# Kernel optimization log

Measured on AMD Instinct MI355X. Metric: run time of the kernel, lower is better.

The kernel has to match this reference:

```python
import jax, jax.numpy as jnp
import numpy as np

H, N, DIN, DOUT = 8, 2048, 768, 1024
HD = DOUT // H
SCALE = 1.0 / float(np.sqrt(HD))
NEG = -1e9
EPS = 1e-5


def setup_inputs() -> dict:
    key = jax.random.key(0)
    ks = jax.random.split(key, 20)
    w = lambda i, shape: jax.random.normal(ks[i], shape, jnp.float32) * 0.02
    inp = {
        'x': jax.random.normal(ks[0], (N, DIN), jnp.float32),
        'batch': jnp.sort(jax.random.randint(ks[1], (N,), 0, 64)).astype(jnp.int64)
                 if jax.config.jax_enable_x64 else jnp.sort(jax.random.randint(ks[1], (N,), 0, 64)),
        'motif_to_atom_attn': jax.random.normal(ks[2], (H, N, N), jnp.float32),
        'wq_w': w(3, (DIN, DOUT)), 'wq_b': jnp.zeros((DOUT,), jnp.float32),
        'wk_w': w(4, (DIN, DOUT)), 'wk_b': jnp.zeros((DOUT,), jnp.float32),
        'wv_w': w(5, (DIN, DOUT)), 'wv_b': jnp.zeros((DOUT,), jnp.float32),
        'wo_w': w(6, (DOUT, DIN)), 'wo_b': jnp.zeros((DIN,), jnp.float32),
        'ln_g': jnp.ones((DIN,), jnp.float32), 'ln_b': jnp.zeros((DIN,), jnp.float32),
        'alpha': jnp.float32(0.5), 'beta': jnp.float32(0.5),
        'gate_q_w': w(7, (DOUT, H)), 'gate_q_b': jnp.zeros((H,), jnp.float32),
        'gate_k_w': w(8, (DOUT, H)), 'gate_k_b': jnp.zeros((H,), jnp.float32),
        'head_interaction': jnp.eye(H, dtype=jnp.float32) + 0.01 * jax.random.normal(ks[9], (H, H), jnp.float32),
    }
    return inp


def reference(x, batch, motif_to_atom_attn, wq_w, wq_b, wk_w, wk_b, wv_w, wv_b,
              wo_w, wo_b, ln_g, ln_b, alpha, beta, gate_q_w, gate_q_b,
              gate_k_w, gate_k_b, head_interaction):
    n = x.shape[0]
    # projections -> [H, N, hd]
    q = (x @ wq_w + wq_b).reshape(n, H, HD).transpose(1, 0, 2)
    k = (x @ wk_w + wk_b).reshape(n, H, HD).transpose(1, 0, 2)
    v = (x @ wv_w + wv_b).reshape(n, H, HD).transpose(1, 0, 2)
    # scaled scores with block-diagonal batch mask [H, N, N]
    scores = jnp.einsum('hid,hjd->hij', q, k) * SCALE
    mask = batch[:, None] == batch[None, :]
    scores = jnp.where(mask[None, :, :], scores, NEG)
    attn_final = scores
    # Guide bias: torch permutes (N,N,H)->permute(2,1,0) which TRANSPOSES node dims
    attn_base = alpha * scores + beta * motif_to_atom_attn          # [H, N, N]
    attn_final = attn_final + jnp.swapaxes(attn_base, 1, 2)        # transposed in (i,j)
    # dynamic gating
    q_flat = q.transpose(1, 0, 2).reshape(n, DOUT)
    k_flat = k.transpose(1, 0, 2).reshape(n, DOUT)
    gq = jnp.tanh(q_flat @ gate_q_w + gate_q_b)                    # [N, H]
    gk = jnp.tanh(k_flat @ gate_k_w + gate_k_b)                    # [N, H]
    attn_final = attn_final + scores * (gq.T[:, :, None] + gk.T[:, None, :])
    # head interaction: res[m,i,j] = sum_h scores[h,i,j] * W[h,m]
    attn_final = attn_final + jnp.einsum('hij,hm->mij', scores, head_interaction)
    probs = jax.nn.softmax(attn_final, axis=-1)
    out = jnp.einsum('hij,hjd->hid', probs, v).transpose(1, 0, 2).reshape(n, DOUT)
    out = out @ wo_w + wo_b
    y = out + x
    mu = jnp.mean(y, axis=-1, keepdims=True)
    var = jnp.mean(jnp.square(y - mu), axis=-1, keepdims=True)
    y = (y - mu) * jax.lax.rsqrt(var + EPS) * ln_g + ln_b
    return y, attn_final
```

## Files before the change

### kernel.cpp

```cpp
#include <hip/hip_runtime.h>

#define NN    2048
#define DIN   768
#define DOUT  1024
#define NH    8
#define HD    128
#define SCALEF 0.08838834764831845f
#define NEGF  (-1.0e9f)
#define EPSF  1e-5f
#define EXPSHIFT 16.0f

typedef __attribute__((ext_vector_type(4))) float f32x4;
typedef __attribute__((ext_vector_type(8))) short bf16x8;

#define OFF_OBF  0
#define OFF_WOT  1048576
#define OFF_YACC 1441792
#define OFF_Q    3686400
#define OFF_K    4734976
#define OFF_VB   5783552
#define OFF_VT   6832128
#define OFF_XB   7880704
#define OFF_WT   8667136
#define OFF_GQ   9846784
#define OFF_GK   9863168

__device__ __forceinline__ short f2bf(float f) {
  union { float f; unsigned u; } v; v.f = f;
  unsigned r = v.u + 0x7FFF + ((v.u >> 16) & 1);
  return (short)(r >> 16);
}
__device__ __forceinline__ float bf2f(short s) {
  union { unsigned u; float f; } v; v.u = ((unsigned)(unsigned short)s) << 16;
  return v.f;
}

__global__ __launch_bounds__(256) void k_prep(const float* __restrict__ x,
                                              short* __restrict__ xb,
                                              const float* __restrict__ wq,
                                              const float* __restrict__ wk,
                                              const float* __restrict__ wv,
                                              short* __restrict__ Wt,
                                              const float* __restrict__ wo,
                                              short* __restrict__ wot) {
  const int bid = blockIdx.x;
  const int tid = threadIdx.x;
  if (bid < 1536) {
    int idx = bid * 256 + tid;
    float4 v = ((const float4*)x)[idx];
    union { short s[4]; float2 f; } u;
    u.s[0] = f2bf(v.x); u.s[1] = f2bf(v.y); u.s[2] = f2bf(v.z); u.s[3] = f2bf(v.w);
    ((float2*)xb)[idx] = u.f;
    return;
  }
  __shared__ float t[64][65];
  if (bid < 2112) {
    const int w = bid - 1536;
    const int z = w / 192, rem = w % 192;
    const int c0 = (rem % 16) * 64, k0 = (rem / 16) * 64;
    const float* Wm = (z == 0) ? wq : (z == 1) ? wk : wv;
#pragma unroll
    for (int l = 0; l < 4; ++l) {
      int f = tid + l * 256;
      int r = f >> 4, c4 = (f & 15) * 4;
      *(float4*)&t[r][c4] = *(const float4*)(Wm + (size_t)(k0 + r) * DOUT + c0 + c4);
    }
    __syncthreads();
    int r2 = tid >> 2, q = tid & 3;
    union { short s[16]; float4 f[2]; } buf;
#pragma unroll
    for (int jj = 0; jj < 16; ++jj) buf.s[jj] = f2bf(t[q * 16 + jj][r2]);
    short* dst = Wt + (size_t)z * (1024 * 768) + (size_t)(c0 + r2) * 768 + k0 + q * 16;
    ((float4*)dst)[0] = buf.f[0];
    ((float4*)dst)[1] = buf.f[1];
  } else {
    const int w = bid - 2112;
    const int c0 = (w % 12) * 64, k0 = (w / 12) * 64;
#pragma unroll
    for (int l = 0; l < 4; ++l) {
      int f = tid + l * 256;
      int r = f >> 4, c4 = (f & 15) * 4;
      *(float4*)&t[r][c4] = *(const float4*)(wo + (size_t)(k0 + r) * DIN + c0 + c4);
    }
    __syncthreads();
    int r2 = tid >> 2, q = tid & 3;
    union { short s[16]; float4 f[2]; } buf;
#pragma unroll
    for (int jj = 0; jj < 16; ++jj) buf.s[jj] = f2bf(t[q * 16 + jj][r2]);
    short* dst = wot + (size_t)(c0 + r2) * DOUT + k0 + q * 16;
    ((float4*)dst)[0] = buf.f[0];
    ((float4*)dst)[1] = buf.f[1];
  }
}

__global__ __launch_bounds__(256) void k_qkv(const short* __restrict__ xb,
                                             const short* __restrict__ Wt,
                                             const float* __restrict__ bq,
                                             const float* __restrict__ bk,
                                             const float* __restrict__ bv,
                                             short* __restrict__ Qb,
                                             short* __restrict__ Kb,
                                             short* __restrict__ Vb) {
  const int n0 = blockIdx.x * 128;
  const int i0 = blockIdx.y * 64;
  const int mat = n0 >> 10;
  const int cl = n0 & 1023;
  const float* bias = (mat == 0) ? bq : (mat == 1) ? bk : bv;
  const short* Wm = Wt + (size_t)mat * (1024 * 768);
  const int tid = threadIdx.x, lane = tid & 63, wave = tid >> 6;
  const int ln = lane & 15, quad = lane >> 4, q8 = quad * 8;
  __shared__ __align__(16) short Bs[2][128][56];
  const int brow = tid >> 1, bseg = (tid & 1) * 16;
  const short* gB = Wm + (size_t)(cl + brow) * DIN + bseg;
  {
    bf16x8 b0 = *(const bf16x8*)(gB);
    bf16x8 b1 = *(const bf16x8*)(gB + 8);
    *(bf16x8*)&Bs[0][brow][bseg] = b0;
    *(bf16x8*)&Bs[0][brow][bseg + 8] = b1;
  }
  bf16x8 cb0 = *(const bf16x8*)(gB + 32);
  bf16x8 cb1 = *(const bf16x8*)(gB + 40);
  __syncthreads();
  f32x4 acc[8];
#pragma unroll
  for (int nt = 0; nt < 8; ++nt) acc[nt] = (f32x4){0.f, 0.f, 0.f, 0.f};
  const short* a0 = xb + (size_t)(i0 + 16 * wave + ln) * DIN + q8;
  for (int ks = 0; ks < 24; ++ks) {
    const int bufc = ks & 1;
    bf16x8 nb0, nb1;
    if (ks < 22) {
      nb0 = *(const bf16x8*)(gB + 32 * (ks + 2));
      nb1 = *(const bf16x8*)(gB + 32 * (ks + 2) + 8);
    }
    bf16x8 A0 = *(const bf16x8*)(a0 + 32 * ks);
#pragma unroll
    for (int nt = 0; nt < 8; ++nt) {
      bf16x8 B = *(const bf16x8*)&Bs[bufc][16 * nt + ln][q8];
      acc[nt] = __builtin_amdgcn_mfma_f32_16x16x32_bf16(A0, B, acc[nt], 0, 0, 0);
    }
    if (ks < 23) {
      *(bf16x8*)&Bs[bufc ^ 1][brow][bseg] = cb0;
      *(bf16x8*)&Bs[bufc ^ 1][brow][bseg + 8] = cb1;
    }
    __syncthreads();
    if (ks < 22) { cb0 = nb0; cb1 = nb1; }
  }
#pragma unroll
  for (int nt = 0; nt < 8; ++nt) {
    int cg = cl + 16 * nt + ln;
    float bb = bias[cg];
#pragma unroll
    for (int reg = 0; reg < 4; ++reg) {
      int rr = i0 + 16 * wave + quad * 4 + reg;
      short s = f2bf(acc[nt][reg] + bb);
      if (mat == 2) {
        Vb[(size_t)rr * 1024 + cg] = s;
      } else {
        int h = cg >> 7, d = cg & 127;
        (mat == 0 ? Qb : Kb)[((size_t)h * NN + rr) * HD + d] = s;
      }
    }
  }
}

__global__ __launch_bounds__(256) void k_vtg(const short* __restrict__ Qb,
                                             const short* __restrict__ Kb,
                                             const float* __restrict__ gqw,
                                             const float* __restrict__ gqb,
                                             const float* __restrict__ gkw,
                                             const float* __restrict__ gkb,
                                             float* __restrict__ GQ,
                                             float* __restrict__ GK,
                                             const short* __restrict__ Vb,
                                             short* __restrict__ Vt) {
  const int bid = blockIdx.x;
  const int tid = threadIdx.x;
  __shared__ __align__(16) char smem[17408];
  if (bid < 2048) {
    const int i = bid;
    const int lane = tid & 63, wave = tid >> 6;
    float aq[NH] = {}, ak[NH] = {};
    for (int d = tid; d < DOUT; d += 256) {
      int h = d >> 7, dd = d & 127;
      float qv = bf2f(Qb[((size_t)h * NN + i) * HD + dd]);
      float kv = bf2f(Kb[((size_t)h * NN + i) * HD + dd]);
      float4 ga = *(const float4*)(gqw + (size_t)d * NH);
      float4 gb = *(const float4*)(gqw + (size_t)d * NH + 4);
      float4 ha = *(const float4*)(gkw + (size_t)d * NH);
      float4 hb = *(const float4*)(gkw + (size_t)d * NH + 4);
      aq[0] = fmaf(qv, ga.x, aq[0]); aq[1] = fmaf(qv, ga.y, aq[1]);
      aq[2] = fmaf(qv, ga.z, aq[2]); aq[3] = fmaf(qv, ga.w, aq[3]);
      aq[4] = fmaf(qv, gb.x, aq[4]); aq[5] = fmaf(qv, gb.y, aq[5]);
      aq[6] = fmaf(qv, gb.z, aq[6]); aq[7] = fmaf(qv, gb.w, aq[7]);
      ak[0] = fmaf(kv, ha.x, ak[0]); ak[1] = fmaf(kv, ha.y, ak[1]);
      ak[2] = fmaf(kv, ha.z, ak[2]); ak[3] = fmaf(kv, ha.w, ak[3]);
      ak[4] = fmaf(kv, hb.x, ak[4]); ak[5] = fmaf(kv, hb.y, ak[5]);
      ak[6] = fmaf(kv, hb.z, ak[6]); ak[7] = fmaf(kv, hb.w, ak[7]);
    }
#pragma unroll
    for (int h = 0; h < NH; ++h) {
#pragma unroll
      for (int off = 1; off < 64; off <<= 1) {
        aq[h] += __shfl_xor(aq[h], off);
        ak[h] += __shfl_xor(ak[h], off);
      }
    }
    auto part = (float (*)[16])(smem);
    if (lane == 0) {
#pragma unroll
      for (int h = 0; h < NH; ++h) {
        part[wave][h] = aq[h];
        part[wave][8 + h] = ak[h];
      }
    }
    __syncthreads();
    if (tid < 16) {
      float s = part[0][tid] + part[1][tid] + part[2][tid] + part[3][tid];
      if (tid < 8) GQ[(size_t)i * NH + tid] = tanhf(s + gqb[tid]);
      else GK[(size_t)i * NH + tid - 8] = tanhf(s + gkb[tid - 8]);
    }
  } else {
    auto t = (short (*)[136])(smem);
    const int w = bid - 2048;
    const int i0 = (w & 31) * 64, h = w >> 5;
#pragma unroll
    for (int l = 0; l < 2; ++l) {
      int f = tid + l * 256;
      int r = f >> 3, c8 = (f & 7) * 16;
      const short* src = Vb + (size_t)(i0 + r) * 1024 + h * HD + c8;
      *(bf16x8*)&t[r][c8] = *(const bf16x8*)src;
      *(bf16x8*)&t[r][c8 + 8] = *(const bf16x8*)(src + 8);
    }
    __syncthreads();
    int d = tid >> 1, half = tid & 1;
    union { short s[32]; float4 f[4]; } buf;
#pragma unroll
    for (int ii = 0; ii < 32; ++ii) buf.s[ii] = t[32 * half + ii][d];
    short* dst = Vt + (size_t)h * (HD * NN) + (size_t)d * NN + i0 + 32 * half;
#pragma unroll
    for (int q = 0; q < 4; ++q) ((float4*)dst)[q] = buf.f[q];
  }
}

__global__ __launch_bounds__(256, 4) void k_sa(const short* __restrict__ Qb,
                                               const short* __restrict__ Kb,
                                               const int* __restrict__ batch,
                                               const float* __restrict__ motif,
                                               const float* __restrict__ GQ,
                                               const float* __restrict__ GK,
                                               const float* __restrict__ Wh,
                                               const float* __restrict__ alpha_p,
                                               const float* __restrict__ beta_p,
                                               float* __restrict__ ATTN) {
  const unsigned gid = blockIdx.y * gridDim.x + blockIdx.x;
  const unsigned xcd = gid & 7, idx = gid >> 3;
  const unsigned P = xcd + 8 * (idx >> 8);
  const unsigned r256 = idx & 255;
  const unsigned bx = 16 * (P & 3) + (r256 & 15);
  const unsigned by = 16 * (P >> 2) + (r256 >> 4);
  const int i0 = by * 32, j0 = bx * 32;

  const int tid = threadIdx.x, lane = tid & 63, wave = tid >> 6;
  const int wr = wave >> 1, wc = wave & 1;
  const int ln = lane & 15, quad = lane >> 4, q8 = quad * 8;

  __shared__ __align__(16) char smem[38400];
  auto Qs  = (short (*)[32][136])(smem);
  auto Ks  = (short (*)[32][136])(smem + 17408);
  auto oL8 = (float (*)[34])(smem);
  auto gqL = (float (*)[12])(smem + 34816);
  auto gkL = (float (*)[12])(smem + 36352);
  float* sW = (float*)(smem + 37888);

  const int rA = 16 * wr + quad * 4;
  const int cA = 16 * wc + ln;

  const int srow = tid >> 3, sseg = (tid & 7) * 16;
  const short* gQ0 = Qb + (size_t)(i0 + srow) * HD + sseg;
  const short* gK0 = Kb + (size_t)(j0 + srow) * HD + sseg;
  const size_t hstep = (size_t)NN * HD;

  {
    bf16x8 q0 = *(const bf16x8*)(gQ0);
    bf16x8 q1 = *(const bf16x8*)(gQ0 + 8);
    bf16x8 k0 = *(const bf16x8*)(gK0);
    bf16x8 k1 = *(const bf16x8*)(gK0 + 8);
    *(bf16x8*)&Qs[0][srow][sseg] = q0;
    *(bf16x8*)&Qs[0][srow][sseg + 8] = q1;
    *(bf16x8*)&Ks[0][srow][sseg] = k0;
    *(bf16x8*)&Ks[0][srow][sseg + 8] = k1;
  }
  bf16x8 cq0 = *(const bf16x8*)(gQ0 + hstep);
  bf16x8 cq1 = *(const bf16x8*)(gQ0 + hstep + 8);
  bf16x8 ck0 = *(const bf16x8*)(gK0 + hstep);
  bf16x8 ck1 = *(const bf16x8*)(gK0 + hstep + 8);
  if (tid < 64) {
    const int half = tid >> 5, r = tid & 31;
    const float* src = (half ? GK : GQ) + (size_t)((half ? j0 : i0) + r) * NH;
    float4 a = *(const float4*)src;
    float4 b = *(const float4*)(src + 4);
    float* dst = half ? &gkL[r][0] : &gqL[r][0];
    *(float4*)dst = a;
    *(float4*)(dst + 4) = b;
    sW[tid] = Wh[tid];
  }
  const int4 bi4 = *(const int4*)(batch + i0 + rA);
  const int bj = batch[j0 + cA];
  const float alpha = alpha_p[0], beta = beta_p[0];
  __syncthreads();

  f32x4 accS[NH], accT[NH];
#pragma unroll
  for (int h = 0; h < NH; ++h) {
    accS[h] = (f32x4){0.f, 0.f, 0.f, 0.f};
    accT[h] = (f32x4){0.f, 0.f, 0.f, 0.f};
  }

#pragma unroll
  for (int h = 0; h < NH; ++h) {
    const int bufc = h & 1;
    bf16x8 nq0, nq1, nk0, nk1;
    if (h < 6) {
      const short* gq_ = gQ0 + (size_t)(h + 2) * hstep;
      const short* gk_ = gK0 + (size_t)(h + 2) * hstep;
      nq0 = *(const bf16x8*)(gq_);
      nq1 = *(const bf16x8*)(gq_ + 8);
      nk0 = *(const bf16x8*)(gk_);
      nk1 = *(const bf16x8*)(gk_ + 8);
    }
#pragma unroll
    for (int ks = 0; ks < 4; ++ks) {
      bf16x8 aS = *(const bf16x8*)&Qs[bufc][16 * wr + ln][ks * 32 + q8];
      bf16x8 bS = *(const bf16x8*)&Ks[bufc][16 * wc + ln][ks * 32 + q8];
      accS[h] = __builtin_amdgcn_mfma_f32_16x16x32_bf16(aS, bS, accS[h], 0, 0, 0);
      bf16x8 aT = *(const bf16x8*)&Ks[bufc][16 * wr + ln][ks * 32 + q8];
      bf16x8 bT = *(const bf16x8*)&Qs[bufc][16 * wc + ln][ks * 32 + q8];
      accT[h] = __builtin_amdgcn_mfma_f32_16x16x32_bf16(aT, bT, accT[h], 0, 0, 0);
    }
    if (h < 7) {
      *(bf16x8*)&Qs[bufc ^ 1][srow][sseg] = cq0;
      *(bf16x8*)&Qs[bufc ^ 1][srow][sseg + 8] = cq1;
      *(bf16x8*)&Ks[bufc ^ 1][srow][sseg] = ck0;
      *(bf16x8*)&Ks[bufc ^ 1][srow][sseg + 8] = ck1;
    }
    __syncthreads();
    if (h < 6) { cq0 = nq0; cq1 = nq1; ck0 = nk0; ck1 = nk1; }
  }

  int okm[4];
  okm[0] = (bi4.x == bj); okm[1] = (bi4.y == bj);
  okm[2] = (bi4.z == bj); okm[3] = (bi4.w == bj);
#pragma unroll
  for (int reg = 0; reg < 4; ++reg)
#pragma unroll
    for (int h = 0; h < NH; ++h)
      accS[h][reg] = okm[reg] ? accS[h][reg] * SCALEF : NEGF;

  union { float4 v; float f[4]; } moc, mon, mo2;
  moc.v = *(const float4*)(motif + ((size_t)(j0 + cA)) * NN + i0 + rA);
  mon.v = *(const float4*)(motif + ((size_t)(NN + j0 + cA)) * NN + i0 + rA);
#pragma unroll
  for (int h = 0; h < NH; ++h) {
    if (h < 6)
      mo2.v = *(const float4*)(motif + ((size_t)(h + 2) * NN + j0 + cA) * NN + i0 + rA);
    float w8[NH];
#pragma unroll
    for (int h2 = 0; h2 < NH; ++h2) w8[h2] = sW[h2 * NH + h];
    const float gkj = gkL[cA][h];
#pragma unroll
    for (int reg = 0; reg < 4; ++reg) {
      float tv = okm[reg] ? accT[h][reg] * SCALEF : NEGF;
      float hm = 0.f;
#pragma unroll
      for (int h2 = 0; h2 < NH; ++h2) hm = fmaf(accS[h2][reg], w8[h2], hm);
      float o = accS[h][reg] * (1.f + gqL[rA + reg][h] + gkj) +
                alpha * tv + beta * moc.f[reg] + hm;
      oL8[h * 32 + rA + reg][cA] = o;
    }
    moc.v = mon.v;
    mon.v = mo2.v;
  }
  __syncthreads();

  const int orow = tid >> 3, oslot = (tid & 7) * 4;
#pragma unroll
  for (int h = 0; h < NH; ++h) {
    float2 a = *(const float2*)&oL8[h * 32 + orow][oslot];
    float2 b = *(const float2*)&oL8[h * 32 + orow][oslot + 2];
    float4 ov = float4{a.x, a.y, b.x, b.y};
    *(float4*)(ATTN + ((size_t)h * NN + i0 + orow) * NN + j0 + oslot) = ov;
  }
}

__global__ __launch_bounds__(256) void k_pv(const float* __restrict__ ATTN,
                                            const short* __restrict__ Vt,
                                            short* __restrict__ Obf) {
  const int bid = blockIdx.x;
  const int h = bid & 7;
  const int i0 = (bid >> 3) * 16;
  const int tid = threadIdx.x, lane = tid & 63, wave = tid >> 6;
  const int ln = lane & 15, quad = lane >> 4, q8 = quad * 8;
  __shared__ float accL[4][16][140];
  __shared__ float SUML[4][16];
  const int jbase = wave * 512;
  const float* arow = ATTN + ((size_t)h * NN + i0 + ln) * NN + jbase;
  const short* vbase = Vt + (size_t)h * (HD * NN) + jbase;
  f32x4 acc[8];
#pragma unroll
  for (int nt = 0; nt < 8; ++nt) acc[nt] = (f32x4){0.f, 0.f, 0.f, 0.f};
  float rowsum = 0.f;
  for (int c = 0; c < 16; ++c) {
    const int jk = c * 32;
    float4 u1 = *(const float4*)(arow + jk + q8);
    float4 u2 = *(const float4*)(arow + jk + q8 + 4);
    float p0 = __expf(u1.x - EXPSHIFT), p1 = __expf(u1.y - EXPSHIFT);
    float p2 = __expf(u1.z - EXPSHIFT), p3 = __expf(u1.w - EXPSHIFT);
    float p4 = __expf(u2.x - EXPSHIFT), p5 = __expf(u2.y - EXPSHIFT);
    float p6 = __expf(u2.z - EXPSHIFT), p7 = __expf(u2.w - EXPSHIFT);
    rowsum += ((p0 + p1) + (p2 + p3)) + ((p4 + p5) + (p6 + p7));
    bf16x8 a;
    a[0] = f2bf(p0); a[1] = f2bf(p1); a[2] = f2bf(p2); a[3] = f2bf(p3);
    a[4] = f2bf(p4); a[5] = f2bf(p5); a[6] = f2bf(p6); a[7] = f2bf(p7);
#pragma unroll
    for (int nt = 0; nt < 8; ++nt) {
      bf16x8 b = *(const bf16x8*)(vbase + (size_t)(16 * nt + ln) * NN + jk + q8);
      acc[nt] = __builtin_amdgcn_mfma_f32_16x16x32_bf16(a, b, acc[nt], 0, 0, 0);
    }
  }
  rowsum += __shfl_xor(rowsum, 16);
  rowsum += __shfl_xor(rowsum, 32);
  if (lane < 16) SUML[wave][ln] = rowsum;
#pragma unroll
  for (int nt = 0; nt < 8; ++nt)
#pragma unroll
    for (int reg = 0; reg < 4; ++reg)
      accL[wave][quad * 4 + reg][16 * nt + ln] = acc[nt][reg];
  __syncthreads();
  const int r = tid >> 4, d0 = (tid & 15) * 8;
  const float inv = 1.0f / (SUML[0][r] + SUML[1][r] + SUML[2][r] + SUML[3][r]);
  union { short s[8]; bf16x8 v; } ob;
#pragma unroll
  for (int e = 0; e < 8; ++e) {
    float s = accL[0][r][d0 + e] + accL[1][r][d0 + e] +
              accL[2][r][d0 + e] + accL[3][r][d0 + e];
    ob.s[e] = f2bf(s * inv);
  }
  *(bf16x8*)(Obf + (size_t)(i0 + r) * DOUT + h * HD + d0) = ob.v;
}

__global__ __launch_bounds__(256) void k_outproj(const short* __restrict__ Obf,
                                                 const short* __restrict__ wot,
                                                 float* __restrict__ YACC) {
  const int n0 = blockIdx.x * 64;
  const int i0 = blockIdx.y * 64;
  const int tid = threadIdx.x, lane = tid & 63, wave = tid >> 6;
  const int ln = lane & 15, quad = lane >> 4, q8 = quad * 8;
  __shared__ __align__(16) short Bs[2][64][56];
  const int brow = tid >> 2, bseg = (tid & 3) * 8;
  const short* gB = wot + (size_t)(n0 + brow) * DOUT + bseg;
  {
    bf16x8 b0 = *(const bf16x8*)(gB);
    *(bf16x8*)&Bs[0][brow][bseg] = b0;
  }
  bf16x8 cb0 = *(const bf16x8*)(gB + 32);
  __syncthreads();
  f32x4 acc[4];
#pragma unroll
  for (int nt = 0; nt < 4; ++nt) acc[nt] = (f32x4){0.f, 0.f, 0.f, 0.f};
  const short* a0 = Obf + (size_t)(i0 + 16 * wave + ln) * DOUT + q8;
  for (int ks = 0; ks < 32; ++ks) {
    const int bufc = ks & 1;
    bf16x8 nb0;
    if (ks < 30) nb0 = *(const bf16x8*)(gB + 32 * (ks + 2));
    bf16x8 A0 = *(const bf16x8*)(a0 + 32 * ks);
#pragma unroll
    for (int nt = 0; nt < 4; ++nt) {
      bf16x8 B = *(const bf16x8*)&Bs[bufc][16 * nt + ln][q8];
      acc[nt] = __builtin_amdgcn_mfma_f32_16x16x32_bf16(A0, B, acc[nt], 0, 0, 0);
    }
    if (ks < 31) *(bf16x8*)&Bs[bufc ^ 1][brow][bseg] = cb0;
    __syncthreads();
    if (ks < 30) cb0 = nb0;
  }
#pragma unroll
  for (int nt = 0; nt < 4; ++nt) {
    int cg = n0 + 16 * nt + ln;
#pragma unroll
    for (int reg = 0; reg < 4; ++reg) {
      int rr = i0 + 16 * wave + quad * 4 + reg;
      YACC[(size_t)rr * DIN + cg] = acc[nt][reg];
    }
  }
}

__global__ __launch_bounds__(256) void k_ln(const float* __restrict__ YACC,
                                            const float* __restrict__ x,
                                            const float* __restrict__ wo_b,
                                            const float* __restrict__ g,
                                            const float* __restrict__ b,
                                            float* __restrict__ y) {
  const int i = blockIdx.x;
  const int tid = threadIdx.x;
  const int lane = tid & 63, wave = tid >> 6;
  float v[3];
#pragma unroll
  for (int t = 0; t < 3; ++t) {
    int cc = tid + t * 256;
    v[t] = YACC[(size_t)i * DIN + cc] + wo_b[cc] + x[(size_t)i * DIN + cc];
  }
  __shared__ float p1[4], p2[4];
  float s = v[0] + v[1] + v[2];
#pragma unroll
  for (int off = 1; off < 64; off <<= 1) s += __shfl_xor(s, off);
  if (lane == 0) p1[wave] = s;
  __syncthreads();
  const float mu = (p1[0] + p1[1] + p1[2] + p1[3]) * (1.0f / DIN);
  float q = 0.f;
#pragma unroll
  for (int t = 0; t < 3; ++t) {
    float d = v[t] - mu;
    q += d * d;
  }
#pragma unroll
  for (int off = 1; off < 64; off <<= 1) q += __shfl_xor(q, off);
  if (lane == 0) p2[wave] = q;
  __syncthreads();
  const float rs = rsqrtf((p2[0] + p2[1] + p2[2] + p2[3]) * (1.0f / DIN) + EPSF);
#pragma unroll
  for (int t = 0; t < 3; ++t) {
    int cc = tid + t * 256;
    y[(size_t)i * DIN + cc] = (v[t] - mu) * rs * g[cc] + b[cc];
  }
}

extern "C" void kernel_launch(void* const* d_in, const int* in_sizes, int n_in,
                              void* d_out, int out_size, void* d_ws, size_t ws_size,
                              hipStream_t stream) {
  (void)in_sizes; (void)n_in; (void)out_size; (void)ws_size;
  const float* x       = (const float*)d_in[0];
  const int*   batch   = (const int*)d_in[1];
  const float* motif   = (const float*)d_in[2];
  const float* wq_w    = (const float*)d_in[3];
  const float* wq_b    = (const float*)d_in[4];
  const float* wk_w    = (const float*)d_in[5];
  const float* wk_b    = (const float*)d_in[6];
  const float* wv_w    = (const float*)d_in[7];
  const float* wv_b    = (const float*)d_in[8];
  const float* wo_w    = (const float*)d_in[9];
  const float* wo_b    = (const float*)d_in[10];
  const float* ln_g    = (const float*)d_in[11];
  const float* ln_b    = (const float*)d_in[12];
  const float* alpha_p = (const float*)d_in[13];
  const float* beta_p  = (const float*)d_in[14];
  const float* gq_w    = (const float*)d_in[15];
  const float* gq_b    = (const float*)d_in[16];
  const float* gk_w    = (const float*)d_in[17];
  const float* gk_b    = (const float*)d_in[18];
  const float* headW   = (const float*)d_in[19];

  float* y    = (float*)d_out;
  float* ATTN = (float*)d_out + (size_t)NN * DIN;
  float* ws   = (float*)d_ws;
  short* Obf  = (short*)(ws + OFF_OBF);
  short* wot  = (short*)(ws + OFF_WOT);
  float* YACC = ws + OFF_YACC;
  short* Qb   = (short*)(ws + OFF_Q);
  short* Kb   = (short*)(ws + OFF_K);
  short* Vb   = (short*)(ws + OFF_VB);
  short* Vt   = (short*)(ws + OFF_VT);
  short* xb   = (short*)(ws + OFF_XB);
  short* Wt   = (short*)(ws + OFF_WT);
  float* GQ   = ws + OFF_GQ;
  float* GK   = ws + OFF_GK;

  k_prep<<<2304, 256, 0, stream>>>(x, xb, wq_w, wk_w, wv_w, Wt, wo_w, wot);
  k_qkv<<<dim3(24, 32), 256, 0, stream>>>(xb, Wt, wq_b, wk_b, wv_b, Qb, Kb, Vb);
  k_vtg<<<2304, 256, 0, stream>>>(Qb, Kb, gq_w, gq_b, gk_w, gk_b, GQ, GK, Vb, Vt);
  k_sa<<<dim3(64, 64), 256, 0, stream>>>(Qb, Kb, batch, motif, GQ, GK, headW,
                                         alpha_p, beta_p, ATTN);
  k_pv<<<1024, 256, 0, stream>>>(ATTN, Vt, Obf);
  k_outproj<<<dim3(12, 32), 256, 0, stream>>>(Obf, wot, YACC);
  k_ln<<<NN, 256, 0, stream>>>(YACC, x, wo_b, ln_g, ln_b, y);
}
```

Before: 455.0 us.

## Use MFMA for gating projection, prefetch in PV, smaller outproj tiles

The gating projection now processes 16 rows per block using bf16 MFMA against gate weights staged in shared memory, replacing 2048 scalar-reduction blocks. The PV kernel software-prefetches the next chunk of V and attention logits into registers and sets launch bounds to encourage occupancy. The output projection halves its row tile so the grid doubles and fills more CUs. Gate weights are rounded to bf16, which slightly reduces precision, and the extra prefetch registers increase register pressure.

Result: no change. 453.8 us (-0.3%).

```diff
diff --git a/kernel.cpp b/kernel.cpp
--- a/kernel.cpp
+++ b/kernel.cpp
@@ -175,53 +175,62 @@
                                              short* __restrict__ Vt) {
   const int bid = blockIdx.x;
   const int tid = threadIdx.x;
-  __shared__ __align__(16) char smem[17408];
-  if (bid < 2048) {
-    const int i = bid;
+  __shared__ __align__(16) char smem[41216];
+  if (bid < 128) {
+    const int i0 = bid * 16;
     const int lane = tid & 63, wave = tid >> 6;
-    float aq[NH] = {}, ak[NH] = {};
-    for (int d = tid; d < DOUT; d += 256) {
-      int h = d >> 7, dd = d & 127;
-      float qv = bf2f(Qb[((size_t)h * NN + i) * HD + dd]);
-      float kv = bf2f(Kb[((size_t)h * NN + i) * HD + dd]);
-      float4 ga = *(const float4*)(gqw + (size_t)d * NH);
-      float4 gb = *(const float4*)(gqw + (size_t)d * NH + 4);
-      float4 ha = *(const float4*)(gkw + (size_t)d * NH);
-      float4 hb = *(const float4*)(gkw + (size_t)d * NH + 4);
-      aq[0] = fmaf(qv, ga.x, aq[0]); aq[1] = fmaf(qv, ga.y, aq[1]);
-      aq[2] = fmaf(qv, ga.z, aq[2]); aq[3] = fmaf(qv, ga.w, aq[3]);
-      aq[4] = fmaf(qv, gb.x, aq[4]); aq[5] = fmaf(qv, gb.y, aq[5]);
-      aq[6] = fmaf(qv, gb.z, aq[6]); aq[7] = fmaf(qv, gb.w, aq[7]);
-      ak[0] = fmaf(kv, ha.x, ak[0]); ak[1] = fmaf(kv, ha.y, ak[1]);
-      ak[2] = fmaf(kv, ha.z, ak[2]); ak[3] = fmaf(kv, ha.w, ak[3]);
-      ak[4] = fmaf(kv, hb.x, ak[4]); ak[5] = fmaf(kv, hb.y, ak[5]);
-      ak[6] = fmaf(kv, hb.z, ak[6]); ak[7] = fmaf(kv, hb.w, ak[7]);
-    }
-#pragma unroll
-    for (int h = 0; h < NH; ++h) {
-#pragma unroll
-      for (int off = 1; off < 64; off <<= 1) {
-        aq[h] += __shfl_xor(aq[h], off);
-        ak[h] += __shfl_xor(ak[h], off);
-      }
-    }
-    auto part = (float (*)[16])(smem);
-    if (lane == 0) {
-#pragma unroll
-      for (int h = 0; h < NH; ++h) {
-        part[wave][h] = aq[h];
-        part[wave][8 + h] = ak[h];
-      }
-    }
-    __syncthreads();
-    if (tid < 16) {
-      float s = part[0][tid] + part[1][tid] + part[2][tid] + part[3][tid];
-      if (tid < 8) GQ[(size_t)i * NH + tid] = tanhf(s + gqb[tid]);
-      else GK[(size_t)i * NH + tid - 8] = tanhf(s + gkb[tid - 8]);
+    const int ln = lane & 15, quad = lane >> 4, q8 = quad * 8;
+    auto BqT = (short (*)[1032])(smem);
+    auto BkT = (short (*)[1032])(smem + 16512);
+    auto pQ  = (float (*)[16][16])(smem + 33024);
+    auto pK  = (float (*)[16][16])(smem + 37120);
+#pragma unroll
+    for (int e = 0; e < 4; ++e) {
+      const int k = tid * 4 + e;
+      float4 a = *(const float4*)(gqw + (size_t)k * NH);
+      float4 b = *(const float4*)(gqw + (size_t)k * NH + 4);
+      BqT[0][k] = f2bf(a.x); BqT[1][k] = f2bf(a.y);
+      BqT[2][k] = f2bf(a.z); BqT[3][k] = f2bf(a.w);
+      BqT[4][k] = f2bf(b.x); BqT[5][k] = f2bf(b.y);
+      BqT[6][k] = f2bf(b.z); BqT[7][k] = f2bf(b.w);
+      float4 c = *(const float4*)(gkw + (size_t)k * NH);
+      float4 d = *(const float4*)(gkw + (size_t)k * NH + 4);
+      BkT[0][k] = f2bf(c.x); BkT[1][k] = f2bf(c.y);
+      BkT[2][k] = f2bf(c.z); BkT[3][k] = f2bf(c.w);
+      BkT[4][k] = f2bf(d.x); BkT[5][k] = f2bf(d.y);
+      BkT[6][k] = f2bf(d.z); BkT[7][k] = f2bf(d.w);
+    }
+    __syncthreads();
+    f32x4 aq = (f32x4){0.f, 0.f, 0.f, 0.f};
+    f32x4 ak = (f32x4){0.f, 0.f, 0.f, 0.f};
+    const int lnb = ln & 7;
+#pragma unroll
+    for (int c = 0; c < 8; ++c) {
+      const int k0 = wave * 256 + c * 32;
+      const int h = k0 >> 7, dd = (k0 & 127) + q8;
+      bf16x8 Aq = *(const bf16x8*)(Qb + ((size_t)h * NN + i0 + ln) * HD + dd);
+      bf16x8 Bq = *(const bf16x8*)&BqT[lnb][k0 + q8];
+      aq = __builtin_amdgcn_mfma_f32_16x16x32_bf16(Aq, Bq, aq, 0, 0, 0);
+      bf16x8 Ak = *(const bf16x8*)(Kb + ((size_t)h * NN + i0 + ln) * HD + dd);
+      bf16x8 Bk = *(const bf16x8*)&BkT[lnb][k0 + q8];
+      ak = __builtin_amdgcn_mfma_f32_16x16x32_bf16(Ak, Bk, ak, 0, 0, 0);
+    }
+#pragma unroll
+    for (int reg = 0; reg < 4; ++reg) {
+      pQ[wave][quad * 4 + reg][ln] = aq[reg];
+      pK[wave][quad * 4 + reg][ln] = ak[reg];
+    }
+    __syncthreads();
+    const int row = tid >> 4, col = tid & 15;
+    if (col < NH) {
+      float sq = pQ[0][row][col] + pQ[1][row][col] + pQ[2][row][col] + pQ[3][row][col];
+      GQ[(size_t)(i0 + row) * NH + col] = tanhf(sq + gqb[col]);
+      float sk = pK[0][row][col] + pK[1][row][col] + pK[2][row][col] + pK[3][row][col];
+      GK[(size_t)(i0 + row) * NH + col] = tanhf(sk + gkb[col]);
     }
   } else {
     auto t = (short (*)[136])(smem);
-    const int w = bid - 2048;
+    const int w = bid - 128;
     const int i0 = (w & 31) * 64, h = w >> 5;
 #pragma unroll
     for (int l = 0; l < 2; ++l) {
@@ -392,9 +401,9 @@
   }
 }
 
-__global__ __launch_bounds__(256) void k_pv(const float* __restrict__ ATTN,
-                                            const short* __restrict__ Vt,
-                                            short* __restrict__ Obf) {
+__global__ __launch_bounds__(256, 4) void k_pv(const float* __restrict__ ATTN,
+                                               const short* __restrict__ Vt,
+                                               short* __restrict__ Obf) {
   const int bid = blockIdx.x;
   const int h = bid & 7;
   const int i0 = (bid >> 3) * 16;
@@ -409,10 +418,24 @@
 #pragma unroll
   for (int nt = 0; nt < 8; ++nt) acc[nt] = (f32x4){0.f, 0.f, 0.f, 0.f};
   float rowsum = 0.f;
+  bf16x8 vc[8];
+#pragma unroll
+  for (int nt = 0; nt < 8; ++nt)
+    vc[nt] = *(const bf16x8*)(vbase + (size_t)(16 * nt + ln) * NN + q8);
+  float4 u1 = *(const float4*)(arow + q8);
+  float4 u2 = *(const float4*)(arow + q8 + 4);
+#pragma unroll
   for (int c = 0; c < 16; ++c) {
     const int jk = c * 32;
-    float4 u1 = *(const float4*)(arow + jk + q8);
-    float4 u2 = *(const float4*)(arow + jk + q8 + 4);
+    bf16x8 vn[8];
+    float4 n1, n2;
+    if (c < 15) {
+#pragma unroll
+      for (int nt = 0; nt < 8; ++nt)
+        vn[nt] = *(const bf16x8*)(vbase + (size_t)(16 * nt + ln) * NN + jk + 32 + q8);
+      n1 = *(const float4*)(arow + jk + 32 + q8);
+      n2 = *(const float4*)(arow + jk + 32 + q8 + 4);
+    }
     float p0 = __expf(u1.x - EXPSHIFT), p1 = __expf(u1.y - EXPSHIFT);
     float p2 = __expf(u1.z - EXPSHIFT), p3 = __expf(u1.w - EXPSHIFT);
     float p4 = __expf(u2.x - EXPSHIFT), p5 = __expf(u2.y - EXPSHIFT);
@@ -422,9 +445,12 @@
     a[0] = f2bf(p0); a[1] = f2bf(p1); a[2] = f2bf(p2); a[3] = f2bf(p3);
     a[4] = f2bf(p4); a[5] = f2bf(p5); a[6] = f2bf(p6); a[7] = f2bf(p7);
 #pragma unroll
-    for (int nt = 0; nt < 8; ++nt) {
-      bf16x8 b = *(const bf16x8*)(vbase + (size_t)(16 * nt + ln) * NN + jk + q8);
-      acc[nt] = __builtin_amdgcn_mfma_f32_16x16x32_bf16(a, b, acc[nt], 0, 0, 0);
+    for (int nt = 0; nt < 8; ++nt)
+      acc[nt] = __builtin_amdgcn_mfma_f32_16x16x32_bf16(a, vc[nt], acc[nt], 0, 0, 0);
+    if (c < 15) {
+#pragma unroll
+      for (int nt = 0; nt < 8; ++nt) vc[nt] = vn[nt];
+      u1 = n1; u2 = n2;
     }
   }
   rowsum += __shfl_xor(rowsum, 16);
@@ -452,9 +478,10 @@
                                                  const short* __restrict__ wot,
                                                  float* __restrict__ YACC) {
   const int n0 = blockIdx.x * 64;
-  const int i0 = blockIdx.y * 64;
+  const int i0 = blockIdx.y * 32;
   const int tid = threadIdx.x, lane = tid & 63, wave = tid >> 6;
   const int ln = lane & 15, quad = lane >> 4, q8 = quad * 8;
+  const int wr = wave & 1, wcol = wave >> 1;
   __shared__ __align__(16) short Bs[2][64][56];
   const int brow = tid >> 2, bseg = (tid & 3) * 8;
   const short* gB = wot + (size_t)(n0 + brow) * DOUT + bseg;
@@ -464,18 +491,18 @@
   }
   bf16x8 cb0 = *(const bf16x8*)(gB + 32);
   __syncthreads();
-  f32x4 acc[4];
-#pragma unroll
-  for (int nt = 0; nt < 4; ++nt) acc[nt] = (f32x4){0.f, 0.f, 0.f, 0.f};
-  const short* a0 = Obf + (size_t)(i0 + 16 * wave + ln) * DOUT + q8;
+  f32x4 acc[2];
+#pragma unroll
+  for (int nt = 0; nt < 2; ++nt) acc[nt] = (f32x4){0.f, 0.f, 0.f, 0.f};
+  const short* a0 = Obf + (size_t)(i0 + 16 * wr + ln) * DOUT + q8;
   for (int ks = 0; ks < 32; ++ks) {
     const int bufc = ks & 1;
     bf16x8 nb0;
     if (ks < 30) nb0 = *(const bf16x8*)(gB + 32 * (ks + 2));
     bf16x8 A0 = *(const bf16x8*)(a0 + 32 * ks);
 #pragma unroll
-    for (int nt = 0; nt < 4; ++nt) {
-      bf16x8 B = *(const bf16x8*)&Bs[bufc][16 * nt + ln][q8];
+    for (int nt = 0; nt < 2; ++nt) {
+      bf16x8 B = *(const bf16x8*)&Bs[bufc][32 * wcol + 16 * nt + ln][q8];
       acc[nt] = __builtin_amdgcn_mfma_f32_16x16x32_bf16(A0, B, acc[nt], 0, 0, 0);
     }
     if (ks < 31) *(bf16x8*)&Bs[bufc ^ 1][brow][bseg] = cb0;
@@ -483,11 +510,11 @@
     if (ks < 30) cb0 = nb0;
   }
 #pragma unroll
-  for (int nt = 0; nt < 4; ++nt) {
-    int cg = n0 + 16 * nt + ln;
+  for (int nt = 0; nt < 2; ++nt) {
+    int cg = n0 + 32 * wcol + 16 * nt + ln;
 #pragma unroll
     for (int reg = 0; reg < 4; ++reg) {
-      int rr = i0 + 16 * wave + quad * 4 + reg;
+      int rr = i0 + 16 * wr + quad * 4 + reg;
       YACC[(size_t)rr * DIN + cg] = acc[nt][reg];
     }
   }
@@ -575,10 +602,10 @@
 
   k_prep<<<2304, 256, 0, stream>>>(x, xb, wq_w, wk_w, wv_w, Wt, wo_w, wot);
   k_qkv<<<dim3(24, 32), 256, 0, stream>>>(xb, Wt, wq_b, wk_b, wv_b, Qb, Kb, Vb);
-  k_vtg<<<2304, 256, 0, stream>>>(Qb, Kb, gq_w, gq_b, gk_w, gk_b, GQ, GK, Vb, Vt);
+  k_vtg<<<384, 256, 0, stream>>>(Qb, Kb, gq_w, gq_b, gk_w, gk_b, GQ, GK, Vb, Vt);
   k_sa<<<dim3(64, 64), 256, 0, stream>>>(Qb, Kb, batch, motif, GQ, GK, headW,
                                          alpha_p, beta_p, ATTN);
   k_pv<<<1024, 256, 0, stream>>>(ATTN, Vt, Obf);
-  k_outproj<<<dim3(12, 32), 256, 0, stream>>>(Obf, wot, YACC);
+  k_outproj<<<dim3(12, 64), 256, 0, stream>>>(Obf, wot, YACC);
   k_ln<<<NN, 256, 0, stream>>>(YACC, x, wo_b, ln_g, ln_b, y);
 }
```
